# Kernel tuning notes

Hardware: AMD Instinct MI355X
Metric: run time of the kernel (lower is better)

## Reference

```python
import jax, jax.numpy as jnp
import numpy as np

B, S, SE, D, H, DFF = 2, 2048, 2048, 512, 8, 2048
DEPTH = D // H  # per-head depth


def setup_inputs() -> dict:
    key = jax.random.key(0)
    ks = jax.random.split(key, 16)
    def w(k, shape, s=0.02):
        return jax.random.normal(k, shape, jnp.float32) * s
    inp = {
        "x": jax.random.normal(ks[0], (B, S, D), jnp.float32),
        "enc_output": jax.random.normal(ks[1], (B, SE, D), jnp.float32),
        # causal look-ahead mask: 1 where attention is disallowed
        "look_ahead_mask": jnp.triu(jnp.ones((S, S), jnp.float32), k=1)[None, None],
        "padding_mask": jnp.zeros((B, 1, 1, SE), jnp.float32),
    }
    # mha1 (self) and mha2 (cross) projection weights
    for i, pre in enumerate(["mha1", "mha2"]):
        for j, nm in enumerate(["q", "k", "v", "o"]):
            inp[f"{pre}_w{nm}"] = w(ks[2 + i * 4 + j], (D, D))
            inp[f"{pre}_b{nm}"] = jnp.zeros((D,), jnp.float32)
    inp["ffn_w1"] = w(ks[10], (D, DFF))
    inp["ffn_b1"] = jnp.zeros((DFF,), jnp.float32)
    inp["ffn_w2"] = w(ks[11], (DFF, D))
    inp["ffn_b2"] = jnp.zeros((D,), jnp.float32)
    for i in (1, 2, 3):
        inp[f"ln{i}_g"] = jnp.ones((D,), jnp.float32)
        inp[f"ln{i}_b"] = jnp.zeros((D,), jnp.float32)
    return inp


def _split_heads(x):
    b, s, _ = x.shape
    return x.reshape(b, s, H, DEPTH).transpose(0, 2, 1, 3)  # (b,h,s,d)


def _mha(v, k, q, wq, bq, wk, bk, wv, bv, wo, bo, mask):
    b, sq, _ = q.shape
    qh = _split_heads(q @ wq + bq)
    kh = _split_heads(k @ wk + bk)
    vh = _split_heads(v @ wv + bv)
    logits = jnp.einsum("bhqd,bhkd->bhqk", qh, kh) / jnp.sqrt(jnp.float32(DEPTH))
    if mask is not None:
        logits = logits + mask * (-1e9)
    attn = jax.nn.softmax(logits, axis=-1)
    out = jnp.einsum("bhqk,bhkd->bhqd", attn, vh)
    out = out.transpose(0, 2, 1, 3).reshape(b, sq, D)
    return out @ wo + bo


def _ln(x, g, b, eps=1e-6):
    m = x.mean(-1, keepdims=True)
    v = ((x - m) ** 2).mean(-1, keepdims=True)
    return (x - m) / jnp.sqrt(v + eps) * g + b


def reference(x, enc_output, look_ahead_mask, padding_mask,
              mha1_wq, mha1_bq, mha1_wk, mha1_bk, mha1_wv, mha1_bv, mha1_wo, mha1_bo,
              mha2_wq, mha2_bq, mha2_wk, mha2_bk, mha2_wv, mha2_bv, mha2_wo, mha2_bo,
              ffn_w1, ffn_b1, ffn_w2, ffn_b2,
              ln1_g, ln1_b, ln2_g, ln2_b, ln3_g, ln3_b):
    # masked self-attention (dropout is identity at inference)
    attn1 = _mha(x, x, x, mha1_wq, mha1_bq, mha1_wk, mha1_bk, mha1_wv, mha1_bv,
                 mha1_wo, mha1_bo, look_ahead_mask)
    out1 = _ln(attn1 + x, ln1_g, ln1_b)
    # cross-attention: v=k=enc_output, q=out1
    attn2 = _mha(enc_output, enc_output, out1, mha2_wq, mha2_bq, mha2_wk, mha2_bk,
                 mha2_wv, mha2_bv, mha2_wo, mha2_bo, padding_mask)
    out2 = _ln(attn2 + out1, ln2_g, ln2_b)
    ffn = jax.nn.relu(out2 @ ffn_w1 + ffn_b1) @ ffn_w2 + ffn_b2
    return _ln(ffn + out2, ln3_g, ln3_b)
```

## Files before the change

### kernel.cpp

```cpp
#include <hip/hip_runtime.h>
#include <stdint.h>

#define NT 4096
#define SQ 2048
#define DM 512

typedef __attribute__((ext_vector_type(4))) float          f32x4_t;
typedef __attribute__((ext_vector_type(8))) short          bf16x8_t;
typedef __attribute__((ext_vector_type(8))) unsigned short u16x8_t;

#define QSCALE 0.18033688011112042f

__device__ __forceinline__ unsigned short f2bf(float f) {
  unsigned int u = __float_as_uint(f);
  u = u + 0x7FFFu + ((u >> 16) & 1u);
  return (unsigned short)(u >> 16);
}
__device__ __forceinline__ float bf2f(unsigned short u) {
  return __uint_as_float((unsigned int)u << 16);
}
__device__ __forceinline__ unsigned int cvtpk(float lo, float hi) {
  unsigned int r;
  asm("v_cvt_pk_bf16_f32 %0, %1, %2" : "=v"(r) : "v"(lo), "v"(hi));
  return r;
}
__device__ __forceinline__ float exp2fast(float x) {
  float r;
  asm("v_exp_f32 %0, %1" : "=v"(r) : "v"(x));
  return r;
}

__device__ __forceinline__ void gload16(const void* g, void* l) {
  __builtin_amdgcn_global_load_lds(
      (__attribute__((address_space(1))) void*)(g),
      (__attribute__((address_space(3))) void*)(l), 16, 0, 0);
}

#define MFMA16(A, B, C) __builtin_amdgcn_mfma_f32_16x16x32_bf16((A), (B), (C), 0, 0, 0)

__global__ void __launch_bounds__(256) prep_all(
    const float* xs, unsigned short* xd, const float* es, unsigned short* ed,
    const float* s0, const float* s1, const float* s2, const float* s3,
    const float* s4, const float* s5, const float* s6, const float* s7,
    unsigned short* d0, unsigned short* d1, unsigned short* d2, unsigned short* d3,
    unsigned short* d4, unsigned short* d5, unsigned short* d6, unsigned short* d7,
    const float* fw1, unsigned short* w1t, const float* fw2, unsigned short* w2t,
    const float* q1, const float* k1, const float* v1,
    const float* q2, const float* k2, const float* v2,
    float* bqkv1, float* bq2, float* bkv2) {
  __shared__ float t[32][33];
  const int bid = blockIdx.x, tid = threadIdx.x;
  if (bid < 2048) {
    const float* src = bid < 1024 ? xs : es;
    unsigned short* dst = bid < 1024 ? xd : ed;
    int i = ((bid & 1023) * 256 + tid) * 8;
    f32x4_t a = *(const f32x4_t*)(src + i);
    f32x4_t b = *(const f32x4_t*)(src + i + 4);
    u16x8_t o;
    o[0]=f2bf(a[0]); o[1]=f2bf(a[1]); o[2]=f2bf(a[2]); o[3]=f2bf(a[3]);
    o[4]=f2bf(b[0]); o[5]=f2bf(b[1]); o[6]=f2bf(b[2]); o[7]=f2bf(b[3]);
    *(u16x8_t*)(dst + i) = o;
    return;
  }
  if (bid < 6144) {
    const float* src; unsigned short* dst; float scale = 1.f;
    int Ksz, Nsz, n0, k0;
    if (bid < 4096) {
      int tt = bid - 2048, z = tt >> 8, w = tt & 255;
      Ksz = 512; Nsz = 512; n0 = (w & 15) * 32; k0 = (w >> 4) * 32;
      switch (z) {
        case 0: src = s0; dst = d0; scale = QSCALE; break;
        case 1: src = s1; dst = d1; break;
        case 2: src = s2; dst = d2; break;
        case 3: src = s3; dst = d3; break;
        case 4: src = s4; dst = d4; scale = QSCALE; break;
        case 5: src = s5; dst = d5; break;
        case 6: src = s6; dst = d6; break;
        default: src = s7; dst = d7; break;
      }
    } else if (bid < 5120) {
      int tt = bid - 4096;
      src = fw1; dst = w1t; Ksz = 512; Nsz = 2048;
      n0 = (tt & 63) * 32; k0 = (tt >> 6) * 32;
    } else {
      int tt = bid - 5120;
      src = fw2; dst = w2t; Ksz = 2048; Nsz = 512;
      n0 = (tt & 15) * 32; k0 = (tt >> 4) * 32;
    }
    int tx = tid & 31, ty = tid >> 5;
#pragma unroll
    for (int i = 0; i < 4; i++)
      t[ty + 8*i][tx] = src[(size_t)(k0 + ty + 8*i) * Nsz + n0 + tx];
    __syncthreads();
#pragma unroll
    for (int i = 0; i < 4; i++)
      dst[(size_t)(n0 + ty + 8*i) * Ksz + k0 + tx] = f2bf(t[tx][ty + 8*i] * scale);
    return;
  }
  {
    int i = (bid - 6144) * 256 + tid;
    int seg = i >> 9, off = i & 511;
    switch (seg) {
      case 0: bqkv1[off]        = q1[off] * QSCALE; break;
      case 1: bqkv1[512 + off]  = k1[off]; break;
      case 2: bqkv1[1024 + off] = v1[off]; break;
      case 3: bq2[off]          = q2[off] * QSCALE; break;
      case 4: bkv2[off]         = k2[off]; break;
      default: bkv2[512 + off]  = v2[off]; break;
    }
  }
}

__global__ void __launch_bounds__(256) vtrans(const unsigned short* __restrict__ src, int lds_,
                                              int coloff, unsigned short* __restrict__ dst, int Skv) {
  __shared__ unsigned short t[64][65];
  int st = blockIdx.x * 64, bh = blockIdx.y;
  int b = bh >> 3, h = bh & 7;
  int tid = threadIdx.x;
  const unsigned short* s = src + ((size_t)b * Skv + st) * lds_ + coloff + h * 64;
#pragma unroll
  for (int i = 0; i < 16; i++) {
    int e = i * 256 + tid; int r = e >> 6, d = e & 63;
    t[r][d] = s[(size_t)r * lds_ + d];
  }
  __syncthreads();
  unsigned short* dp = dst + (size_t)bh * 64 * Skv + st;
#pragma unroll
  for (int i = 0; i < 2; i++) {
    int e = i * 256 + tid;
    int d = e >> 3, rc = (e & 7) * 8;
    u16x8_t o;
#pragma unroll
    for (int k = 0; k < 8; k++) o[k] = t[rc + k][d];
    *(u16x8_t*)(dp + (size_t)d * Skv + rc) = o;
  }
}

template <int BM, int BN, int EPI>
__global__ void __launch_bounds__(256) gemm_bt(const unsigned short* __restrict__ A, int lda,
                                               const unsigned short* __restrict__ Bt, int ldb,
                                               const float* __restrict__ bias,
                                               void* __restrict__ Cv, int ldc, int K) {
  constexpr int WM = BM / 2, WN = BN / 2, FM = WM / 16, FN = WN / 16;
  constexpr int ITA = BM * 8 / 256, ITB = BN * 8 / 256;
  constexpr int ABY = BM * 128, BBY = BN * 128;
  __shared__ __align__(16) unsigned short ldsA[2][BM * 64];
  __shared__ __align__(16) unsigned short ldsB[2][BN * 64];
  const int tid = threadIdx.x;
  const int lane = tid & 63, wave = tid >> 6;
  const int wr = wave >> 1, wc = wave & 1;
  const int l15 = lane & 15, l4 = lane >> 4;
  const long brow = (long)blockIdx.x * BM;
  const long bcol = (long)blockIdx.y * BN;

  const unsigned short* ag[ITA]; unsigned int al[ITA];
  const unsigned short* bg[ITB]; unsigned int bl[ITB];
#pragma unroll
  for (int i = 0; i < ITA; i++) {
    int L = tid + 256 * i, row = L >> 3, c = L & 7, g = c ^ (row & 7);
    ag[i] = A + (brow + row) * (long)lda + g * 8;
    al[i] = (unsigned int)L * 16;
  }
#pragma unroll
  for (int i = 0; i < ITB; i++) {
    int L = tid + 256 * i, row = L >> 3, c = L & 7, g = c ^ (row & 7);
    bg[i] = Bt + (bcol + row) * (long)ldb + g * 8;
    bl[i] = (unsigned int)L * 16;
  }

  unsigned int aoff[FM][2], boff[FN][2];
#pragma unroll
  for (int m = 0; m < FM; m++)
#pragma unroll
    for (int kk = 0; kk < 2; kk++) {
      int row = wr * WM + m * 16 + l15;
      aoff[m][kk] = (unsigned int)row * 128 + ((((unsigned)(kk * 4 + l4)) ^ (unsigned)(row & 7)) << 4);
    }
#pragma unroll
  for (int n = 0; n < FN; n++)
#pragma unroll
    for (int kk = 0; kk < 2; kk++) {
      int col = wc * WN + n * 16 + l15;
      boff[n][kk] = (unsigned int)col * 128 + ((((unsigned)(kk * 4 + l4)) ^ (unsigned)(col & 7)) << 4);
    }

  f32x4_t acc[FM][FN] = {};
  const int nt = K >> 6;

#pragma unroll
  for (int i = 0; i < ITA; i++) { gload16(ag[i], (char*)ldsA[0] + al[i]); ag[i] += 64; }
#pragma unroll
  for (int i = 0; i < ITB; i++) { gload16(bg[i], (char*)ldsB[0] + bl[i]); bg[i] += 64; }
  __syncthreads();

  int cur = 0;
  for (int t = 0; t < nt; ++t) {
    if (t + 1 < nt) {
      unsigned int da = (cur ^ 1) * ABY, db = (cur ^ 1) * BBY;
#pragma unroll
      for (int i = 0; i < ITA; i++) { gload16(ag[i], (char*)ldsA[0] + da + al[i]); ag[i] += 64; }
#pragma unroll
      for (int i = 0; i < ITB; i++) { gload16(bg[i], (char*)ldsB[0] + db + bl[i]); bg[i] += 64; }
    }
    const char* pa = (const char*)ldsA[0] + cur * ABY;
    const char* pb = (const char*)ldsB[0] + cur * BBY;
#pragma unroll
    for (int kk = 0; kk < 2; kk++) {
      bf16x8_t af[FM], bfr[FN];
#pragma unroll
      for (int m = 0; m < FM; m++) af[m] = *(const bf16x8_t*)(pa + aoff[m][kk]);
#pragma unroll
      for (int n = 0; n < FN; n++) bfr[n] = *(const bf16x8_t*)(pb + boff[n][kk]);
#pragma unroll
      for (int m = 0; m < FM; m++)
#pragma unroll
        for (int n = 0; n < FN; n++)
          acc[m][n] = MFMA16(af[m], bfr[n], acc[m][n]);
    }
    __syncthreads();
    cur ^= 1;
  }

#pragma unroll
  for (int m = 0; m < FM; m++)
#pragma unroll
    for (int n = 0; n < FN; n++) {
      long col = bcol + wc * WN + n * 16 + l15;
      float bv = bias[col];
#pragma unroll
      for (int j = 0; j < 4; j++) {
        long row = brow + wr * WM + m * 16 + l4 * 4 + j;
        float v = acc[m][n][j] + bv;
        if (EPI == 1) v = fmaxf(v, 0.f);
        if (EPI == 2) ((float*)Cv)[row * ldc + col] = v;
        else          ((unsigned short*)Cv)[row * ldc + col] = f2bf(v);
      }
    }
}

template <int BM, int BN>
__global__ void __launch_bounds__(256) gemm_btk(const unsigned short* __restrict__ A, int lda,
                                                const unsigned short* __restrict__ Bt, int ldb,
                                                float* __restrict__ Cp, int ldc, int Kchunk) {
  constexpr int WM = BM / 2, WN = BN / 2, FM = WM / 16, FN = WN / 16;
  constexpr int ITA = BM * 8 / 256, ITB = BN * 8 / 256;
  constexpr int ABY = BM * 128, BBY = BN * 128;
  __shared__ __align__(16) unsigned short ldsA[2][BM * 64];
  __shared__ __align__(16) unsigned short ldsB[2][BN * 64];
  const int tid = threadIdx.x;
  const int lane = tid & 63, wave = tid >> 6;
  const int wr = wave >> 1, wc = wave & 1;
  const int l15 = lane & 15, l4 = lane >> 4;
  const long brow = (long)blockIdx.x * BM;
  const long bcol = (long)blockIdx.y * BN;
  const int koff = blockIdx.z * Kchunk;

  const unsigned short* ag[ITA]; unsigned int al[ITA];
  const unsigned short* bg[ITB]; unsigned int bl[ITB];
#pragma unroll
  for (int i = 0; i < ITA; i++) {
    int L = tid + 256 * i, row = L >> 3, c = L & 7, g = c ^ (row & 7);
    ag[i] = A + (brow + row) * (long)lda + koff + g * 8;
    al[i] = (unsigned int)L * 16;
  }
#pragma unroll
  for (int i = 0; i < ITB; i++) {
    int L = tid + 256 * i, row = L >> 3, c = L & 7, g = c ^ (row & 7);
    bg[i] = Bt + (bcol + row) * (long)ldb + koff + g * 8;
    bl[i] = (unsigned int)L * 16;
  }

  unsigned int aoff[FM][2], boff[FN][2];
#pragma unroll
  for (int m = 0; m < FM; m++)
#pragma unroll
    for (int kk = 0; kk < 2; kk++) {
      int row = wr * WM + m * 16 + l15;
      aoff[m][kk] = (unsigned int)row * 128 + ((((unsigned)(kk * 4 + l4)) ^ (unsigned)(row & 7)) << 4);
    }
#pragma unroll
  for (int n = 0; n < FN; n++)
#pragma unroll
    for (int kk = 0; kk < 2; kk++) {
      int col = wc * WN + n * 16 + l15;
      boff[n][kk] = (unsigned int)col * 128 + ((((unsigned)(kk * 4 + l4)) ^ (unsigned)(col & 7)) << 4);
    }

  f32x4_t acc[FM][FN] = {};
  const int nt = Kchunk >> 6;

#pragma unroll
  for (int i = 0; i < ITA; i++) { gload16(ag[i], (char*)ldsA[0] + al[i]); ag[i] += 64; }
#pragma unroll
  for (int i = 0; i < ITB; i++) { gload16(bg[i], (char*)ldsB[0] + bl[i]); bg[i] += 64; }
  __syncthreads();

  int cur = 0;
  for (int t = 0; t < nt; ++t) {
    if (t + 1 < nt) {
      unsigned int da = (cur ^ 1) * ABY, db = (cur ^ 1) * BBY;
#pragma unroll
      for (int i = 0; i < ITA; i++) { gload16(ag[i], (char*)ldsA[0] + da + al[i]); ag[i] += 64; }
#pragma unroll
      for (int i = 0; i < ITB; i++) { gload16(bg[i], (char*)ldsB[0] + db + bl[i]); bg[i] += 64; }
    }
    const char* pa = (const char*)ldsA[0] + cur * ABY;
    const char* pb = (const char*)ldsB[0] + cur * BBY;
#pragma unroll
    for (int kk = 0; kk < 2; kk++) {
      bf16x8_t af[FM], bfr[FN];
#pragma unroll
      for (int m = 0; m < FM; m++) af[m] = *(const bf16x8_t*)(pa + aoff[m][kk]);
#pragma unroll
      for (int n = 0; n < FN; n++) bfr[n] = *(const bf16x8_t*)(pb + boff[n][kk]);
#pragma unroll
      for (int m = 0; m < FM; m++)
#pragma unroll
        for (int n = 0; n < FN; n++)
          acc[m][n] = MFMA16(af[m], bfr[n], acc[m][n]);
    }
    __syncthreads();
    cur ^= 1;
  }

  float* cp = Cp + (size_t)blockIdx.z * NT * DM;
#pragma unroll
  for (int m = 0; m < FM; m++)
#pragma unroll
    for (int n = 0; n < FN; n++) {
      long col = bcol + wc * WN + n * 16 + l15;
#pragma unroll
      for (int j = 0; j < 4; j++) {
        long row = brow + wr * WM + m * 16 + l4 * 4 + j;
        cp[row * ldc + col] = acc[m][n][j];
      }
    }
}

template <bool CAUSAL, int C>
__global__ void __launch_bounds__(512, 6) attn_part(const unsigned short* __restrict__ Q, int ldq, int qc0,
                                                    const unsigned short* __restrict__ Kb, int ldk, int kc0,
                                                    const unsigned short* __restrict__ Vt,
                                                    unsigned short* __restrict__ obuf,
                                                    float* __restrict__ lbuf, int Skv) {
  __shared__ __align__(16) unsigned short kt[2][4096];
  __shared__ __align__(16) unsigned short vt[2][4096];
  const int qt = blockIdx.x, bh = blockIdx.y, cch = blockIdx.z;
  const int b = bh >> 3, h = bh & 7;
  const int tid = threadIdx.x, wave = tid >> 6, lane = tid & 63;
  const int sub = wave >> 2, wrow = wave & 3;
  const int l15 = lane & 15, l4 = lane >> 4, q7 = l15 & 7;
  const long qrow0 = (long)b * SQ + qt * 128 + sub * 64;
  const long krow0 = (long)b * Skv;
  const unsigned short* vtb = Vt + (size_t)bh * 64 * Skv;
  const int qoff = qc0 + h * 64, koff = kc0 + h * 64;

  const int ntt = CAUSAL ? (2 * qt + 2) : (Skv >> 6);
  const int t0 = (ntt * cch) / C, t1 = (ntt * (cch + 1)) / C;

  bf16x8_t qf[2];
  {
    long qr = qrow0 + wrow * 16 + l15;
    const unsigned short* qp = Q + qr * (long)ldq + qoff + l4 * 8;
    qf[0] = *(const bf16x8_t*)(qp);
    qf[1] = *(const bf16x8_t*)(qp + 32);
  }

  const unsigned short* kg; const unsigned short* vg;
  {
    int sr = tid >> 3, scc = tid & 7;
    int ssc = scc ^ (sr & 7);
    int rk = (sr & 0x23) | ((sr & 0x0C) << 1) | ((sr & 0x10) >> 2);
    kg = Kb + (krow0 + t0 * 64 + rk) * (long)ldk + koff + ssc * 8;
    vg = vtb + (size_t)sr * Skv + t0 * 64 + ssc * 8;
  }
  const unsigned int sld = (unsigned int)tid * 16;
  const long kstep = 64 * (long)ldk;

  const unsigned int pbase = (unsigned int)l15 * 128;
  unsigned int xo[2];
  xo[0] = ((unsigned)(l4 ^ q7)) << 4;
  xo[1] = ((unsigned)((4 + l4) ^ q7)) << 4;

  const int qa = qt * 128 + sub * 64 + wrow * 16 + l15;
  const int tdiag = qt * 2 + sub;

  f32x4_t of[4] = {};
  float lrow = 0.f;

  if (t0 < t1) {
    gload16(kg, (char*)kt + sld);
    gload16(vg, (char*)vt + sld);
    kg += kstep; vg += 64;
  }

  int cur = 0;
  for (int t = t0; t < t1; ++t) {
    asm volatile("s_waitcnt vmcnt(0)" ::: "memory");
    __builtin_amdgcn_s_barrier();
    if (t + 1 < t1) {
      unsigned int d = (cur ^ 1) * 8192;
      gload16(kg, (char*)kt + d + sld);
      gload16(vg, (char*)vt + d + sld);
      kg += kstep; vg += 64;
    }
    const char* kbp = (const char*)kt + cur * 8192 + pbase;
    const char* vbp = (const char*)vt + cur * 8192 + pbase;

    f32x4_t sf[4] = {};
    __builtin_amdgcn_s_setprio(1);
#pragma unroll
    for (int n = 0; n < 4; n++) {
      bf16x8_t kf0 = *(const bf16x8_t*)(kbp + xo[0] + n * 2048);
      bf16x8_t kf1 = *(const bf16x8_t*)(kbp + xo[1] + n * 2048);
      sf[n] = MFMA16(kf0, qf[0], sf[n]);
      sf[n] = MFMA16(kf1, qf[1], sf[n]);
    }
    __builtin_amdgcn_s_setprio(0);
    if (CAUSAL && t >= tdiag) {
      int base = (t << 6) + 8 * l4 - qa;
#pragma unroll
      for (int n = 0; n < 4; n++) {
        int kbn = 32 * (n >> 1) + 4 * (n & 1);
#pragma unroll
        for (int j = 0; j < 4; j++)
          if (base + kbn + j > 0) sf[n][j] = -1e30f;
      }
    }
#pragma unroll
    for (int n = 0; n < 4; n++)
#pragma unroll
      for (int j = 0; j < 4; j++) sf[n][j] = exp2fast(sf[n][j]);
    f32x4_t rv = (sf[0] + sf[1]) + (sf[2] + sf[3]);
    lrow += (rv[0] + rv[1]) + (rv[2] + rv[3]);

    union { unsigned int u[4]; bf16x8_t v; } pa0, pa1;
    pa0.u[0] = cvtpk(sf[0][0], sf[0][1]); pa0.u[1] = cvtpk(sf[0][2], sf[0][3]);
    pa0.u[2] = cvtpk(sf[1][0], sf[1][1]); pa0.u[3] = cvtpk(sf[1][2], sf[1][3]);
    pa1.u[0] = cvtpk(sf[2][0], sf[2][1]); pa1.u[1] = cvtpk(sf[2][2], sf[2][3]);
    pa1.u[2] = cvtpk(sf[3][0], sf[3][1]); pa1.u[3] = cvtpk(sf[3][2], sf[3][3]);

    __builtin_amdgcn_s_setprio(1);
#pragma unroll
    for (int n2 = 0; n2 < 4; n2++) {
      bf16x8_t vf0 = *(const bf16x8_t*)(vbp + xo[0] + n2 * 2048);
      bf16x8_t vf1 = *(const bf16x8_t*)(vbp + xo[1] + n2 * 2048);
      of[n2] = MFMA16(pa0.v, vf0, of[n2]);
      of[n2] = MFMA16(pa1.v, vf1, of[n2]);
    }
    __builtin_amdgcn_s_setprio(0);
    cur ^= 1;
  }
  const int blk = (cch * 16 + bh) * 32 + qt * 2 + sub;
  unsigned short* ob = obuf + (size_t)blk * 4096;
#pragma unroll
  for (int j = 0; j < 4; j++) {
    int row = wrow * 16 + l4 * 4 + j;
#pragma unroll
    for (int n2 = 0; n2 < 4; n2++)
      ob[row * 64 + n2 * 16 + l15] = f2bf(of[n2][j]);
  }
  lrow += __shfl_xor(lrow, 16);
  lrow += __shfl_xor(lrow, 32);
  if (l4 == 0) lbuf[(size_t)blk * 64 + wrow * 16 + l15] = lrow;
}

template <int C>
__global__ void __launch_bounds__(256) attn_combine(const unsigned short* __restrict__ obuf,
                                                    const float* __restrict__ lbuf,
                                                    unsigned short* __restrict__ Out) {
  const int qt = blockIdx.x, bh = blockIdx.y;
  const int b = bh >> 3, h = bh & 7;
  const int tid = threadIdx.x;
  const int r = tid >> 2, qd = tid & 3;

  float wsum = 0.f;
#pragma unroll
  for (int c = 0; c < C; c++)
    wsum += lbuf[(size_t)((c * 16 + bh) * 32 + qt) * 64 + r];
  float inv = 1.f / wsum;

  float acc[16] = {};
#pragma unroll
  for (int c = 0; c < C; c++) {
    const unsigned short* op = obuf + ((size_t)((c * 16 + bh) * 32 + qt) * 64 + r) * 64 + qd * 16;
    u16x8_t a = *(const u16x8_t*)(op);
    u16x8_t bv = *(const u16x8_t*)(op + 8);
#pragma unroll
    for (int k = 0; k < 8; k++) {
      acc[k]     += bf2f(a[k]);
      acc[8 + k] += bf2f(bv[k]);
    }
  }
  unsigned short* o = Out + ((size_t)b * SQ + qt * 64 + r) * DM + h * 64 + qd * 16;
#pragma unroll
  for (int k = 0; k < 16; k++) o[k] = f2bf(acc[k] * inv);
}

__global__ void __launch_bounds__(256) ln_kernel(const unsigned short* __restrict__ a, const float* __restrict__ r,
                                                 const float* __restrict__ g, const float* __restrict__ be,
                                                 float* __restrict__ outf, unsigned short* __restrict__ outb) {
  const int wave = threadIdx.x >> 6, lane = threadIdx.x & 63;
  const long row = (long)blockIdx.x * 4 + wave;
  const int off = lane * 8;
  u16x8_t av = *(const u16x8_t*)(a + row * DM + off);
  f32x4_t r0 = *(const f32x4_t*)(r + row * DM + off);
  f32x4_t r1 = *(const f32x4_t*)(r + row * DM + off + 4);
  float v[8];
  float s = 0.f, ss = 0.f;
#pragma unroll
  for (int k = 0; k < 8; k++) {
    v[k] = bf2f(av[k]) + (k < 4 ? r0[k] : r1[k - 4]);
    s += v[k]; ss += v[k] * v[k];
  }
#pragma unroll
  for (int d = 1; d < 64; d <<= 1) { s += __shfl_xor(s, d); ss += __shfl_xor(ss, d); }
  float mean = s * (1.f / 512.f);
  float var = ss * (1.f / 512.f) - mean * mean;
  float rstd = rsqrtf(var + 1e-6f);
  f32x4_t g0 = *(const f32x4_t*)(g + off), g1 = *(const f32x4_t*)(g + off + 4);
  f32x4_t b0 = *(const f32x4_t*)(be + off), b1 = *(const f32x4_t*)(be + off + 4);
  f32x4_t o0, o1; u16x8_t ob;
#pragma unroll
  for (int k = 0; k < 4; k++) {
    o0[k] = (v[k] - mean) * rstd * g0[k] + b0[k];
    o1[k] = (v[k + 4] - mean) * rstd * g1[k] + b1[k];
    ob[k] = f2bf(o0[k]); ob[k + 4] = f2bf(o1[k]);
  }
  *(f32x4_t*)(outf + row * DM + off) = o0;
  *(f32x4_t*)(outf + row * DM + off + 4) = o1;
  if (outb) *(u16x8_t*)(outb + row * DM + off) = ob;
}

__global__ void __launch_bounds__(256) ln_ffn2(const float* __restrict__ pbase,
                                               const float* __restrict__ bias,
                                               const float* __restrict__ resid,
                                               const float* __restrict__ g, const float* __restrict__ be,
                                               float* __restrict__ outf) {
  const int wave = threadIdx.x >> 6, lane = threadIdx.x & 63;
  const long row = (long)blockIdx.x * 4 + wave;
  const size_t stride = (size_t)NT * DM;
  f32x4_t v[2];
  float s = 0.f, ss = 0.f;
#pragma unroll
  for (int i = 0; i < 2; i++) {
    int off = lane * 4 + i * 256;
    size_t idx = row * DM + off;
    f32x4_t xx = *(const f32x4_t*)(pbase + idx);
    xx = xx + *(const f32x4_t*)(pbase + stride + idx);
    xx = xx + *(const f32x4_t*)(bias + off);
    xx = xx + *(const f32x4_t*)(resid + idx);
    v[i] = xx;
    s += xx[0] + xx[1] + xx[2] + xx[3];
    ss += xx[0] * xx[0] + xx[1] * xx[1] + xx[2] * xx[2] + xx[3] * xx[3];
  }
#pragma unroll
  for (int d = 1; d < 64; d <<= 1) { s += __shfl_xor(s, d); ss += __shfl_xor(ss, d); }
  float mean = s * (1.f / 512.f);
  float var = ss * (1.f / 512.f) - mean * mean;
  float rstd = rsqrtf(var + 1e-6f);
#pragma unroll
  for (int i = 0; i < 2; i++)
#pragma unroll
    for (int jj = 0; jj < 4; jj++) {
      int off = lane * 4 + i * 256 + jj;
      outf[row * DM + off] = (v[i][jj] - mean) * rstd * g[off] + be[off];
    }
}

extern "C" void kernel_launch(void* const* d_in, const int* in_sizes, int n_in,
                              void* d_out, int out_size, void* d_ws, size_t ws_size,
                              hipStream_t stream) {
  (void)in_sizes; (void)n_in; (void)out_size;
  const float* x   = (const float*)d_in[0];
  const float* enc = (const float*)d_in[1];
  const float* w1q = (const float*)d_in[4];  const float* b1q = (const float*)d_in[5];
  const float* w1k = (const float*)d_in[6];  const float* b1k = (const float*)d_in[7];
  const float* w1v = (const float*)d_in[8];  const float* b1v = (const float*)d_in[9];
  const float* w1o = (const float*)d_in[10]; const float* b1o = (const float*)d_in[11];
  const float* w2q = (const float*)d_in[12]; const float* b2q = (const float*)d_in[13];
  const float* w2k = (const float*)d_in[14]; const float* b2k = (const float*)d_in[15];
  const float* w2v = (const float*)d_in[16]; const float* b2v = (const float*)d_in[17];
  const float* w2o = (const float*)d_in[18]; const float* b2o = (const float*)d_in[19];
  const float* fw1 = (const float*)d_in[20]; const float* fb1 = (const float*)d_in[21];
  const float* fw2 = (const float*)d_in[22]; const float* fb2 = (const float*)d_in[23];
  const float* g1  = (const float*)d_in[24]; const float* be1 = (const float*)d_in[25];
  const float* g2  = (const float*)d_in[26]; const float* be2 = (const float*)d_in[27];
  const float* g3  = (const float*)d_in[28]; const float* be3 = (const float*)d_in[29];

  char* ws = (char*)d_ws;
  size_t off = 0;
  auto alloc = [&](size_t bytes) -> void* {
    void* p = ws + off;
    off = (off + bytes + 255) & ~(size_t)255;
    return p;
  };
  unsigned short* xb     = (unsigned short*)alloc((size_t)NT * DM * 2);
  unsigned short* eb     = (unsigned short*)alloc((size_t)NT * DM * 2);
  unsigned short* wqkv1t = (unsigned short*)alloc((size_t)1536 * 512 * 2);
  unsigned short* wo1t   = (unsigned short*)alloc((size_t)512 * 512 * 2);
  unsigned short* wq2t   = (unsigned short*)alloc((size_t)512 * 512 * 2);
  unsigned short* wkv2t  = (unsigned short*)alloc((size_t)1024 * 512 * 2);
  unsigned short* wo2t   = (unsigned short*)alloc((size_t)512 * 512 * 2);
  unsigned short* w1t    = (unsigned short*)alloc((size_t)2048 * 512 * 2);
  unsigned short* w2t    = (unsigned short*)alloc((size_t)512 * 2048 * 2);
  float* bqkv1 = (float*)alloc(1536 * 4);
  float* bq2s  = (float*)alloc(512 * 4);
  float* bkv2  = (float*)alloc(1024 * 4);
  unsigned short* qkv1  = (unsigned short*)alloc((size_t)NT * 1536 * 2);
  unsigned short* vt1   = (unsigned short*)alloc((size_t)16 * 64 * SQ * 2);
  unsigned short* attn1 = (unsigned short*)alloc((size_t)NT * DM * 2);
  unsigned short* tmpb  = (unsigned short*)alloc((size_t)NT * DM * 2);
  float* out1f = (float*)alloc((size_t)NT * DM * 4);
  unsigned short* out1b = (unsigned short*)alloc((size_t)NT * DM * 2);
  unsigned short* kv2   = (unsigned short*)alloc((size_t)NT * 1024 * 2);
  float* out2f = (float*)alloc((size_t)NT * DM * 4);
  unsigned short* out2b = (unsigned short*)alloc((size_t)NT * DM * 2);
  unsigned short* hbuf  = (unsigned short*)alloc((size_t)NT * 2048 * 2);
  unsigned short* obuf = (unsigned short*)alloc((size_t)2048 * 4096 * 2);
  float*          lbuf = (float*)alloc((size_t)2048 * 64 * 4);
  float*          pbuf = (float*)alloc((size_t)2 * NT * DM * 4);
  unsigned short* q2     = xb;
  unsigned short* vt2    = vt1;
  unsigned short* attn2o = attn1;
  if (off > ws_size) return;

  prep_all<<<6156, 256, 0, stream>>>(
      x, xb, enc, eb,
      w1q, w1k, w1v, w1o, w2q, w2k, w2v, w2o,
      wqkv1t, wqkv1t + 512 * 512, wqkv1t + 1024 * 512, wo1t,
      wq2t, wkv2t, wkv2t + 512 * 512, wo2t,
      fw1, w1t, fw2, w2t,
      b1q, b1k, b1v, b2q, b2k, b2v, bqkv1, bq2s, bkv2);

  gemm_bt<64, 128, 0><<<dim3(64, 12), 256, 0, stream>>>(xb, DM, wqkv1t, 512, bqkv1, qkv1, 1536, 512);
  vtrans<<<dim3(32, 16), 256, 0, stream>>>(qkv1, 1536, 1024, vt1, SQ);
  attn_part<true, 4><<<dim3(16, 16, 4), 512, 0, stream>>>(qkv1, 1536, 0, qkv1, 1536, 512, vt1, obuf, lbuf, SQ);
  attn_combine<4><<<dim3(32, 16), 256, 0, stream>>>(obuf, lbuf, attn1);
  gemm_bt<64, 64, 0><<<dim3(64, 8), 256, 0, stream>>>(attn1, DM, wo1t, 512, b1o, tmpb, DM, 512);
  ln_kernel<<<1024, 256, 0, stream>>>(tmpb, x, g1, be1, out1f, out1b);

  gemm_bt<64, 64, 0><<<dim3(64, 8), 256, 0, stream>>>(out1b, DM, wq2t, 512, bq2s, q2, DM, 512);
  gemm_bt<64, 128, 0><<<dim3(64, 8), 256, 0, stream>>>(eb, DM, wkv2t, 512, bkv2, kv2, 1024, 512);
  vtrans<<<dim3(32, 16), 256, 0, stream>>>(kv2, 1024, 512, vt2, SQ);
  attn_part<false, 4><<<dim3(16, 16, 4), 512, 0, stream>>>(q2, DM, 0, kv2, 1024, 0, vt2, obuf, lbuf, SQ);
  attn_combine<4><<<dim3(32, 16), 256, 0, stream>>>(obuf, lbuf, attn2o);
  gemm_bt<64, 64, 0><<<dim3(64, 8), 256, 0, stream>>>(attn2o, DM, wo2t, 512, b2o, tmpb, DM, 512);
  ln_kernel<<<1024, 256, 0, stream>>>(tmpb, out1f, g2, be2, out2f, out2b);

  gemm_bt<64, 128, 1><<<dim3(64, 16), 256, 0, stream>>>(out2b, DM, w1t, 512, fb1, hbuf, 2048, 512);
  gemm_btk<64, 128><<<dim3(64, 4, 2), 256, 0, stream>>>(hbuf, 2048, w2t, 2048, pbuf, DM, 1024);
  ln_ffn2<<<1024, 256, 0, stream>>>(pbuf, fb2, out2f, g3, be3, (float*)d_out);
}
```

Before: 172.1 us.

## Merge QKV and cross-KV projections, batch V transposes, shrink attention splits and partials

The self-attention QKV projection and the cross-attention KV projection now run in one launch, and the two V transposes are merged into one launch writing separate buffers. The encoder-side work is hoisted ahead of self-attention so it runs in wider grids. The attention KV split count drops from 4 to 3, and the split-K FFN2 partials are stored as bf16 instead of fp32 to cut traffic into the final layernorm. In exchange, a separate vt2 buffer is needed, the split attention has fewer blocks, and the bf16 partial sums lose some precision.

```diff
diff --git a/kernel.cpp b/kernel.cpp
--- a/kernel.cpp
+++ b/kernel.cpp
@@ -111,10 +111,17 @@
   }
 }
 
-__global__ void __launch_bounds__(256) vtrans(const unsigned short* __restrict__ src, int lds_,
-                                              int coloff, unsigned short* __restrict__ dst, int Skv) {
+__global__ void __launch_bounds__(256) vtrans2(const unsigned short* __restrict__ src1, int lds1, int co1,
+                                               unsigned short* __restrict__ dst1,
+                                               const unsigned short* __restrict__ src2, int lds2, int co2,
+                                               unsigned short* __restrict__ dst2, int Skv) {
   __shared__ unsigned short t[64][65];
-  int st = blockIdx.x * 64, bh = blockIdx.y;
+  int st = blockIdx.x * 64, yy = blockIdx.y;
+  const unsigned short* src = yy < 16 ? src1 : src2;
+  unsigned short* dst = yy < 16 ? dst1 : dst2;
+  int lds_ = yy < 16 ? lds1 : lds2;
+  int coloff = yy < 16 ? co1 : co2;
+  int bh = yy & 15;
   int b = bh >> 3, h = bh & 7;
   int tid = threadIdx.x;
   const unsigned short* s = src + ((size_t)b * Skv + st) * lds_ + coloff + h * 64;
@@ -137,21 +144,17 @@
 }
 
 template <int BM, int BN, int EPI>
-__global__ void __launch_bounds__(256) gemm_bt(const unsigned short* __restrict__ A, int lda,
-                                               const unsigned short* __restrict__ Bt, int ldb,
-                                               const float* __restrict__ bias,
-                                               void* __restrict__ Cv, int ldc, int K) {
+__device__ __forceinline__ void gemm_core(const unsigned short* A, int lda,
+                                          const unsigned short* Bt, int ldb,
+                                          const float* bias, void* Cv, int ldc, int K,
+                                          long brow, long bcol, char* ldsA, char* ldsB) {
   constexpr int WM = BM / 2, WN = BN / 2, FM = WM / 16, FN = WN / 16;
   constexpr int ITA = BM * 8 / 256, ITB = BN * 8 / 256;
   constexpr int ABY = BM * 128, BBY = BN * 128;
-  __shared__ __align__(16) unsigned short ldsA[2][BM * 64];
-  __shared__ __align__(16) unsigned short ldsB[2][BN * 64];
   const int tid = threadIdx.x;
   const int lane = tid & 63, wave = tid >> 6;
   const int wr = wave >> 1, wc = wave & 1;
   const int l15 = lane & 15, l4 = lane >> 4;
-  const long brow = (long)blockIdx.x * BM;
-  const long bcol = (long)blockIdx.y * BN;
 
   const unsigned short* ag[ITA]; unsigned int al[ITA];
   const unsigned short* bg[ITB]; unsigned int bl[ITB];
@@ -188,9 +191,9 @@
   const int nt = K >> 6;
 
 #pragma unroll
-  for (int i = 0; i < ITA; i++) { gload16(ag[i], (char*)ldsA[0] + al[i]); ag[i] += 64; }
-#pragma unroll
-  for (int i = 0; i < ITB; i++) { gload16(bg[i], (char*)ldsB[0] + bl[i]); bg[i] += 64; }
+  for (int i = 0; i < ITA; i++) { gload16(ag[i], ldsA + al[i]); ag[i] += 64; }
+#pragma unroll
+  for (int i = 0; i < ITB; i++) { gload16(bg[i], ldsB + bl[i]); bg[i] += 64; }
   __syncthreads();
 
   int cur = 0;
@@ -198,12 +201,12 @@
     if (t + 1 < nt) {
       unsigned int da = (cur ^ 1) * ABY, db = (cur ^ 1) * BBY;
 #pragma unroll
-      for (int i = 0; i < ITA; i++) { gload16(ag[i], (char*)ldsA[0] + da + al[i]); ag[i] += 64; }
-#pragma unroll
-      for (int i = 0; i < ITB; i++) { gload16(bg[i], (char*)ldsB[0] + db + bl[i]); bg[i] += 64; }
-    }
-    const char* pa = (const char*)ldsA[0] + cur * ABY;
-    const char* pb = (const char*)ldsB[0] + cur * BBY;
+      for (int i = 0; i < ITA; i++) { gload16(ag[i], ldsA + da + al[i]); ag[i] += 64; }
+#pragma unroll
+      for (int i = 0; i < ITB; i++) { gload16(bg[i], ldsB + db + bl[i]); bg[i] += 64; }
+    }
+    const char* pa = ldsA + cur * ABY;
+    const char* pb = ldsB + cur * BBY;
 #pragma unroll
     for (int kk = 0; kk < 2; kk++) {
       bf16x8_t af[FM], bfr[FN];
@@ -226,7 +229,7 @@
 #pragma unroll
     for (int n = 0; n < FN; n++) {
       long col = bcol + wc * WN + n * 16 + l15;
-      float bv = bias[col];
+      float bv = (EPI == 3) ? 0.f : bias[col];
 #pragma unroll
       for (int j = 0; j < 4; j++) {
         long row = brow + wr * WM + m * 16 + l4 * 4 + j;
@@ -238,103 +241,45 @@
     }
 }
 
+template <int BM, int BN, int EPI>
+__global__ void __launch_bounds__(256) gemm_bt(const unsigned short* __restrict__ A, int lda,
+                                               const unsigned short* __restrict__ Bt, int ldb,
+                                               const float* __restrict__ bias,
+                                               void* __restrict__ Cv, int ldc, int K) {
+  __shared__ __align__(16) char ldsA[2 * BM * 128];
+  __shared__ __align__(16) char ldsB[2 * BN * 128];
+  gemm_core<BM, BN, EPI>(A, lda, Bt, ldb, bias, Cv, ldc, K,
+                         (long)blockIdx.x * BM, (long)blockIdx.y * BN, ldsA, ldsB);
+}
+
+__global__ void __launch_bounds__(256) gemm_qkvkv(const unsigned short* __restrict__ xb,
+                                                  const unsigned short* __restrict__ eb,
+                                                  const unsigned short* __restrict__ wqkv1t,
+                                                  const unsigned short* __restrict__ wkv2t,
+                                                  const float* __restrict__ bqkv1,
+                                                  const float* __restrict__ bkv2,
+                                                  unsigned short* __restrict__ qkv1,
+                                                  unsigned short* __restrict__ kv2) {
+  __shared__ __align__(16) char ldsA[2 * 64 * 128];
+  __shared__ __align__(16) char ldsB[2 * 128 * 128];
+  const int y = blockIdx.y;
+  if (y < 12)
+    gemm_core<64, 128, 0>(xb, DM, wqkv1t, 512, bqkv1, qkv1, 1536, 512,
+                          (long)blockIdx.x * 64, (long)y * 128, ldsA, ldsB);
+  else
+    gemm_core<64, 128, 0>(eb, DM, wkv2t, 512, bkv2, kv2, 1024, 512,
+                          (long)blockIdx.x * 64, (long)(y - 12) * 128, ldsA, ldsB);
+}
+
 template <int BM, int BN>
 __global__ void __launch_bounds__(256) gemm_btk(const unsigned short* __restrict__ A, int lda,
                                                 const unsigned short* __restrict__ Bt, int ldb,
-                                                float* __restrict__ Cp, int ldc, int Kchunk) {
-  constexpr int WM = BM / 2, WN = BN / 2, FM = WM / 16, FN = WN / 16;
-  constexpr int ITA = BM * 8 / 256, ITB = BN * 8 / 256;
-  constexpr int ABY = BM * 128, BBY = BN * 128;
-  __shared__ __align__(16) unsigned short ldsA[2][BM * 64];
-  __shared__ __align__(16) unsigned short ldsB[2][BN * 64];
-  const int tid = threadIdx.x;
-  const int lane = tid & 63, wave = tid >> 6;
-  const int wr = wave >> 1, wc = wave & 1;
-  const int l15 = lane & 15, l4 = lane >> 4;
-  const long brow = (long)blockIdx.x * BM;
-  const long bcol = (long)blockIdx.y * BN;
-  const int koff = blockIdx.z * Kchunk;
-
-  const unsigned short* ag[ITA]; unsigned int al[ITA];
-  const unsigned short* bg[ITB]; unsigned int bl[ITB];
-#pragma unroll
-  for (int i = 0; i < ITA; i++) {
-    int L = tid + 256 * i, row = L >> 3, c = L & 7, g = c ^ (row & 7);
-    ag[i] = A + (brow + row) * (long)lda + koff + g * 8;
-    al[i] = (unsigned int)L * 16;
-  }
-#pragma unroll
-  for (int i = 0; i < ITB; i++) {
-    int L = tid + 256 * i, row = L >> 3, c = L & 7, g = c ^ (row & 7);
-    bg[i] = Bt + (bcol + row) * (long)ldb + koff + g * 8;
-    bl[i] = (unsigned int)L * 16;
-  }
-
-  unsigned int aoff[FM][2], boff[FN][2];
-#pragma unroll
-  for (int m = 0; m < FM; m++)
-#pragma unroll
-    for (int kk = 0; kk < 2; kk++) {
-      int row = wr * WM + m * 16 + l15;
-      aoff[m][kk] = (unsigned int)row * 128 + ((((unsigned)(kk * 4 + l4)) ^ (unsigned)(row & 7)) << 4);
-    }
-#pragma unroll
-  for (int n = 0; n < FN; n++)
-#pragma unroll
-    for (int kk = 0; kk < 2; kk++) {
-      int col = wc * WN + n * 16 + l15;
-      boff[n][kk] = (unsigned int)col * 128 + ((((unsigned)(kk * 4 + l4)) ^ (unsigned)(col & 7)) << 4);
-    }
-
-  f32x4_t acc[FM][FN] = {};
-  const int nt = Kchunk >> 6;
-
-#pragma unroll
-  for (int i = 0; i < ITA; i++) { gload16(ag[i], (char*)ldsA[0] + al[i]); ag[i] += 64; }
-#pragma unroll
-  for (int i = 0; i < ITB; i++) { gload16(bg[i], (char*)ldsB[0] + bl[i]); bg[i] += 64; }
-  __syncthreads();
-
-  int cur = 0;
-  for (int t = 0; t < nt; ++t) {
-    if (t + 1 < nt) {
-      unsigned int da = (cur ^ 1) * ABY, db = (cur ^ 1) * BBY;
-#pragma unroll
-      for (int i = 0; i < ITA; i++) { gload16(ag[i], (char*)ldsA[0] + da + al[i]); ag[i] += 64; }
-#pragma unroll
-      for (int i = 0; i < ITB; i++) { gload16(bg[i], (char*)ldsB[0] + db + bl[i]); bg[i] += 64; }
-    }
-    const char* pa = (const char*)ldsA[0] + cur * ABY;
-    const char* pb = (const char*)ldsB[0] + cur * BBY;
-#pragma unroll
-    for (int kk = 0; kk < 2; kk++) {
-      bf16x8_t af[FM], bfr[FN];
-#pragma unroll
-      for (int m = 0; m < FM; m++) af[m] = *(const bf16x8_t*)(pa + aoff[m][kk]);
-#pragma unroll
-      for (int n = 0; n < FN; n++) bfr[n] = *(const bf16x8_t*)(pb + boff[n][kk]);
-#pragma unroll
-      for (int m = 0; m < FM; m++)
-#pragma unroll
-        for (int n = 0; n < FN; n++)
-          acc[m][n] = MFMA16(af[m], bfr[n], acc[m][n]);
-    }
-    __syncthreads();
-    cur ^= 1;
-  }
-
-  float* cp = Cp + (size_t)blockIdx.z * NT * DM;
-#pragma unroll
-  for (int m = 0; m < FM; m++)
-#pragma unroll
-    for (int n = 0; n < FN; n++) {
-      long col = bcol + wc * WN + n * 16 + l15;
-#pragma unroll
-      for (int j = 0; j < 4; j++) {
-        long row = brow + wr * WM + m * 16 + l4 * 4 + j;
-        cp[row * ldc + col] = acc[m][n][j];
-      }
-    }
+                                                unsigned short* __restrict__ Cp, int ldc, int Kchunk) {
+  __shared__ __align__(16) char ldsA[2 * BM * 128];
+  __shared__ __align__(16) char ldsB[2 * BN * 128];
+  gemm_core<BM, BN, 3>(A + blockIdx.z * Kchunk, lda, Bt + blockIdx.z * Kchunk, ldb, nullptr,
+                       Cp + (size_t)blockIdx.z * NT * DM, ldc, Kchunk,
+                       (long)blockIdx.x * BM, (long)blockIdx.y * BN, ldsA, ldsB);
 }
 
 template <bool CAUSAL, int C>
@@ -532,7 +477,7 @@
   if (outb) *(u16x8_t*)(outb + row * DM + off) = ob;
 }
 
-__global__ void __launch_bounds__(256) ln_ffn2(const float* __restrict__ pbase,
+__global__ void __launch_bounds__(256) ln_ffn2(const unsigned short* __restrict__ pbase,
                                                const float* __restrict__ bias,
                                                const float* __restrict__ resid,
                                                const float* __restrict__ g, const float* __restrict__ be,
@@ -540,32 +485,34 @@
   const int wave = threadIdx.x >> 6, lane = threadIdx.x & 63;
   const long row = (long)blockIdx.x * 4 + wave;
   const size_t stride = (size_t)NT * DM;
-  f32x4_t v[2];
+  const int off = lane * 8;
+  u16x8_t p0 = *(const u16x8_t*)(pbase + row * DM + off);
+  u16x8_t p1 = *(const u16x8_t*)(pbase + stride + row * DM + off);
+  f32x4_t r0 = *(const f32x4_t*)(resid + row * DM + off);
+  f32x4_t r1 = *(const f32x4_t*)(resid + row * DM + off + 4);
+  f32x4_t b0 = *(const f32x4_t*)(bias + off), b1 = *(const f32x4_t*)(bias + off + 4);
+  float v[8];
   float s = 0.f, ss = 0.f;
 #pragma unroll
-  for (int i = 0; i < 2; i++) {
-    int off = lane * 4 + i * 256;
-    size_t idx = row * DM + off;
-    f32x4_t xx = *(const f32x4_t*)(pbase + idx);
-    xx = xx + *(const f32x4_t*)(pbase + stride + idx);
-    xx = xx + *(const f32x4_t*)(bias + off);
-    xx = xx + *(const f32x4_t*)(resid + idx);
-    v[i] = xx;
-    s += xx[0] + xx[1] + xx[2] + xx[3];
-    ss += xx[0] * xx[0] + xx[1] * xx[1] + xx[2] * xx[2] + xx[3] * xx[3];
+  for (int k = 0; k < 8; k++) {
+    v[k] = bf2f(p0[k]) + bf2f(p1[k]) + (k < 4 ? r0[k] + b0[k] : r1[k - 4] + b1[k - 4]);
+    s += v[k]; ss += v[k] * v[k];
   }
 #pragma unroll
   for (int d = 1; d < 64; d <<= 1) { s += __shfl_xor(s, d); ss += __shfl_xor(ss, d); }
   float mean = s * (1.f / 512.f);
   float var = ss * (1.f / 512.f) - mean * mean;
   float rstd = rsqrtf(var + 1e-6f);
-#pragma unroll
-  for (int i = 0; i < 2; i++)
-#pragma unroll
-    for (int jj = 0; jj < 4; jj++) {
-      int off = lane * 4 + i * 256 + jj;
-      outf[row * DM + off] = (v[i][jj] - mean) * rstd * g[off] + be[off];
-    }
+  f32x4_t g0 = *(const f32x4_t*)(g + off), g1 = *(const f32x4_t*)(g + off + 4);
+  f32x4_t be0 = *(const f32x4_t*)(be + off), be1 = *(const f32x4_t*)(be + off + 4);
+  f32x4_t o0, o1;
+#pragma unroll
+  for (int k = 0; k < 4; k++) {
+    o0[k] = (v[k] - mean) * rstd * g0[k] + be0[k];
+    o1[k] = (v[k + 4] - mean) * rstd * g1[k] + be1[k];
+  }
+  *(f32x4_t*)(outf + row * DM + off) = o0;
+  *(f32x4_t*)(outf + row * DM + off + 4) = o1;
 }
 
 extern "C" void kernel_launch(void* const* d_in, const int* in_sizes, int n_in,
@@ -609,6 +556,7 @@
   float* bkv2  = (float*)alloc(1024 * 4);
   unsigned short* qkv1  = (unsigned short*)alloc((size_t)NT * 1536 * 2);
   unsigned short* vt1   = (unsigned short*)alloc((size_t)16 * 64 * SQ * 2);
+  unsigned short* vt2   = (unsigned short*)alloc((size_t)16 * 64 * SQ * 2);
   unsigned short* attn1 = (unsigned short*)alloc((size_t)NT * DM * 2);
   unsigned short* tmpb  = (unsigned short*)alloc((size_t)NT * DM * 2);
   float* out1f = (float*)alloc((size_t)NT * DM * 4);
@@ -617,11 +565,10 @@
   float* out2f = (float*)alloc((size_t)NT * DM * 4);
   unsigned short* out2b = (unsigned short*)alloc((size_t)NT * DM * 2);
   unsigned short* hbuf  = (unsigned short*)alloc((size_t)NT * 2048 * 2);
-  unsigned short* obuf = (unsigned short*)alloc((size_t)2048 * 4096 * 2);
-  float*          lbuf = (float*)alloc((size_t)2048 * 64 * 4);
-  float*          pbuf = (float*)alloc((size_t)2 * NT * DM * 4);
+  unsigned short* obuf = (unsigned short*)alloc((size_t)1536 * 4096 * 2);
+  float*          lbuf = (float*)alloc((size_t)1536 * 64 * 4);
+  unsigned short* pbuf = (unsigned short*)alloc((size_t)2 * NT * DM * 2);
   unsigned short* q2     = xb;
-  unsigned short* vt2    = vt1;
   unsigned short* attn2o = attn1;
   if (off > ws_size) return;
 
@@ -633,18 +580,17 @@
       fw1, w1t, fw2, w2t,
       b1q, b1k, b1v, b2q, b2k, b2v, bqkv1, bq2s, bkv2);
 
-  gemm_bt<64, 128, 0><<<dim3(64, 12), 256, 0, stream>>>(xb, DM, wqkv1t, 512, bqkv1, qkv1, 1536, 512);
-  vtrans<<<dim3(32, 16), 256, 0, stream>>>(qkv1, 1536, 1024, vt1, SQ);
-  attn_part<true, 4><<<dim3(16, 16, 4), 512, 0, stream>>>(qkv1, 1536, 0, qkv1, 1536, 512, vt1, obuf, lbuf, SQ);
-  attn_combine<4><<<dim3(32, 16), 256, 0, stream>>>(obuf, lbuf, attn1);
+  gemm_qkvkv<<<dim3(64, 20), 256, 0, stream>>>(xb, eb, wqkv1t, wkv2t, bqkv1, bkv2, qkv1, kv2);
+  vtrans2<<<dim3(32, 32), 256, 0, stream>>>(qkv1, 1536, 1024, vt1, kv2, 1024, 512, vt2, SQ);
+
+  attn_part<true, 3><<<dim3(16, 16, 3), 512, 0, stream>>>(qkv1, 1536, 0, qkv1, 1536, 512, vt1, obuf, lbuf, SQ);
+  attn_combine<3><<<dim3(32, 16), 256, 0, stream>>>(obuf, lbuf, attn1);
   gemm_bt<64, 64, 0><<<dim3(64, 8), 256, 0, stream>>>(attn1, DM, wo1t, 512, b1o, tmpb, DM, 512);
   ln_kernel<<<1024, 256, 0, stream>>>(tmpb, x, g1, be1, out1f, out1b);
 
   gemm_bt<64, 64, 0><<<dim3(64, 8), 256, 0, stream>>>(out1b, DM, wq2t, 512, bq2s, q2, DM, 512);
-  gemm_bt<64, 128, 0><<<dim3(64, 8), 256, 0, stream>>>(eb, DM, wkv2t, 512, bkv2, kv2, 1024, 512);
-  vtrans<<<dim3(32, 16), 256, 0, stream>>>(kv2, 1024, 512, vt2, SQ);
-  attn_part<false, 4><<<dim3(16, 16, 4), 512, 0, stream>>>(q2, DM, 0, kv2, 1024, 0, vt2, obuf, lbuf, SQ);
-  attn_combine<4><<<dim3(32, 16), 256, 0, stream>>>(obuf, lbuf, attn2o);
+  attn_part<false, 3><<<dim3(16, 16, 3), 512, 0, stream>>>(q2, DM, 0, kv2, 1024, 0, vt2, obuf, lbuf, SQ);
+  attn_combine<3><<<dim3(32, 16), 256, 0, stream>>>(obuf, lbuf, attn2o);
   gemm_bt<64, 64, 0><<<dim3(64, 8), 256, 0, stream>>>(attn2o, DM, wo2t, 512, b2o, tmpb, DM, 512);
   ln_kernel<<<1024, 256, 0, stream>>>(tmpb, out1f, g2, be2, out2f, out2b);
 
```

New measurement: 162.3 us. -5.7%, faster.
